# Performance work log

Measured on AMD Instinct MI355X. Metric: run time of the kernel, lower is better.

The kernel has to match this reference:

```python
import jax, jax.numpy as jnp
import numpy as np
import math

VOCAB = 32000
HIDDEN = 256
N_HEADS = 8
HEAD_DIM = 32
MAX_LEN = 2048


def _pos_encoding(max_len, d_model, dtype=jnp.float32):
    # Matches PositionalEncoding buffer (even d_model).
    pos = jnp.arange(max_len, dtype=dtype)[:, None]                       # [L,1]
    div = jnp.exp(jnp.arange(0, d_model, 2, dtype=dtype) * (-(math.log(10000.0) / d_model)))
    ang = pos * div                                                        # [L, d/2]
    pe = jnp.zeros((max_len, d_model), dtype=dtype)
    pe = pe.at[:, 0::2].set(jnp.sin(ang))
    pe = pe.at[:, 1::2].set(jnp.cos(ang))
    return pe


def setup_inputs() -> dict:
    key = jax.random.key(0)
    ks = jax.random.split(key, 7)
    B, S = 8, 2047
    s = 0.02
    x = jax.random.randint(ks[0], (B, S), 0, VOCAB + 1, dtype=jnp.int64)
    emb_w = jax.random.normal(ks[1], (VOCAB + 1, HIDDEN), jnp.float32) * s
    wq = jax.random.normal(ks[2], (N_HEADS, HEAD_DIM, HIDDEN), jnp.float32) * s
    wk = jax.random.normal(ks[3], (N_HEADS, HEAD_DIM, HIDDEN), jnp.float32) * s
    wv = jax.random.normal(ks[4], (N_HEADS, HEAD_DIM, HIDDEN), jnp.float32) * s
    wo = jax.random.normal(ks[5], (HIDDEN, N_HEADS * HEAD_DIM), jnp.float32) * s
    wu = jax.random.normal(ks[6], (VOCAB + 1, HIDDEN), jnp.float32) * s
    return {"x": x, "emb_w": emb_w, "wq": wq, "wk": wk, "wv": wv, "wo": wo, "wu": wu}


def reference(x, emb_w, wq, wk, wv, wo, wu):
    B, S = x.shape
    # prepend CLS token (id=2)
    tok = jnp.concatenate([jnp.full((B, 1), 2, dtype=x.dtype), x], axis=1)  # [B, S+1]
    y = emb_w[tok]                                                          # [B, S+1, H]
    y = y + _pos_encoding(S + 1, HIDDEN, y.dtype)
    # batched per-head QKV (nn.Linear: out = in @ W.T)
    q = jnp.einsum('bsh,nkh->bnsk', y, wq)
    k = jnp.einsum('bsh,nkh->bnsk', y, wk)
    v = jnp.einsum('bsh,nkh->bnsk', y, wv)
    scores = jnp.einsum('bnsk,bntk->bnst', q, k) / (HEAD_DIM ** 0.5)        # [B,N,S+1,S+1]
    A = jax.nn.softmax(scores, axis=-1)
    o = jnp.einsum('bnst,bntk->bnsk', A, v)                                 # [B,N,S+1,K]
    o = jnp.transpose(o, (0, 2, 1, 3)).reshape(B, S + 1, N_HEADS * HEAD_DIM)
    att = o @ wo.T + y     # residual inside MultiHeadAttention
    y = att + y            # second residual in MultiHeadTransformerPosEmb.forward
    out = y[:, 0, :] @ wu.T                                                 # [B, VOCAB+1]
    return out
```

## Files before the change

kernel.cpp:

```cpp
#include <hip/hip_runtime.h>
#include <stdint.h>

#define B_   8
#define S_   2047
#define L_   2048
#define H_   256
#define NH_  8
#define HD_  32
#define V_   32001
#define NCH_ 64
#define TCH_ 32

__device__ __forceinline__ float b2f(unsigned short u) {
    union { uint32_t i; float f; } c; c.i = ((uint32_t)u) << 16; return c.f;
}
__device__ __forceinline__ unsigned short f2b(float f) {
    union { float f; uint32_t i; } c; c.f = f;
    uint32_t x = c.i;
    uint32_t r = (x + 0x7fffu + ((x >> 16) & 1u)) >> 16;
    return (unsigned short)r;
}
__device__ __forceinline__ float foldx(float a, int off) {
    return a + __shfl_xor(a, off, 64);
}
__device__ __forceinline__ float sel8(const float a[8], int j) {
    float v = a[0];
    v = (j == 1) ? a[1] : v;
    v = (j == 2) ? a[2] : v;
    v = (j == 3) ? a[3] : v;
    v = (j == 4) ? a[4] : v;
    v = (j == 5) ? a[5] : v;
    v = (j == 6) ? a[6] : v;
    v = (j == 7) ? a[7] : v;
    return v;
}

__global__ __launch_bounds__(256) void k0_prep(const float* __restrict__ emb,
                                               const float* __restrict__ wq,
                                               const float* __restrict__ wk,
                                               float* __restrict__ qk,
                                               float* __restrict__ y0) {
    __shared__ float y0_l[H_];
    __shared__ float q0p[HD_][8];
    __shared__ float q0_l[HD_];
    int n = blockIdx.x, tid = threadIdx.x;
    float v = emb[2 * H_ + tid] + ((tid & 1) ? 1.0f : 0.0f);
    y0_l[tid] = v;
    if (n == 0) y0[tid] = v;
    __syncthreads();
    {
        int k = tid >> 3, part = tid & 7;
        const float* w = wq + (n * HD_ + k) * H_ + part * 32;
        const float* yy = y0_l + part * 32;
        float acc = 0.f;
#pragma unroll
        for (int j = 0; j < 32; ++j) acc += w[j] * yy[j];
        q0p[k][part] = acc;
    }
    __syncthreads();
    if (tid < HD_) {
        float s = 0.f;
#pragma unroll
        for (int j = 0; j < 8; ++j) s += q0p[tid][j];
        q0_l[tid] = s;
    }
    __syncthreads();
    float acc = 0.f;
    for (int k = 0; k < HD_; ++k)
        acc += q0_l[k] * wk[(n * HD_ + k) * H_ + tid];
    qk[n * H_ + tid] = acc * 0.17677669529663687f;
}

__global__ __launch_bounds__(256) void k1_scores(const int* __restrict__ x,
                                                 const float* __restrict__ emb,
                                                 const float* __restrict__ qkw,
                                                 unsigned short* __restrict__ ycache,
                                                 float* __restrict__ Et) {
    int tid  = threadIdx.x;
    int lane = tid & 63;
    int gid  = blockIdx.x * 4 + (tid >> 6);
    int b = gid >> 11, t = gid & (L_ - 1);
    int h0 = lane * 4;

    float4 qr[NH_];
#pragma unroll
    for (int n = 0; n < NH_; ++n)
        qr[n] = *(const float4*)(qkw + n * H_ + h0);

    const float cdiv = 0.07195578414202881f;
    float div0 = __expf(-(float)(lane * 2) * cdiv);
    float div1 = __expf(-(float)(lane * 2 + 1) * cdiv);
    float a0 = (float)t * div0, a1 = (float)t * div1;
    float s0 = __sinf(a0), c0 = __cosf(a0);
    float s1 = __sinf(a1), c1 = __cosf(a1);

    int tok = (t == 0) ? 2 : x[b * S_ + t - 1];
    float4 ev = *(const float4*)(emb + (size_t)tok * H_ + h0);
    float4 y4;
    y4.x = ev.x + s0; y4.y = ev.y + c0; y4.z = ev.z + s1; y4.w = ev.w + c1;
    ushort4 st;
    st.x = f2b(y4.x); st.y = f2b(y4.y); st.z = f2b(y4.z); st.w = f2b(y4.w);
    *(ushort4*)(ycache + ((size_t)gid << 8) + h0) = st;

    float a[NH_];
#pragma unroll
    for (int n = 0; n < NH_; ++n)
        a[n] = qr[n].x * y4.x + qr[n].y * y4.y + qr[n].z * y4.z + qr[n].w * y4.w;
    float m4[4];
#pragma unroll
    for (int k = 0; k < 4; ++k) {
        float lo = foldx(a[k], 32), hi = foldx(a[k + 4], 32);
        m4[k] = (lane & 32) ? hi : lo;
    }
    float m2[2];
#pragma unroll
    for (int k = 0; k < 2; ++k) {
        float lo = foldx(m4[k], 16), hi = foldx(m4[k + 2], 16);
        m2[k] = (lane & 16) ? hi : lo;
    }
    float lo = foldx(m2[0], 8), hi = foldx(m2[1], 8);
    float m1 = (lane & 8) ? hi : lo;
    m1 = foldx(m1, 4); m1 = foldx(m1, 2); m1 = foldx(m1, 1);
    float e = __expf(m1);
    if ((lane & 7) == 0)
        Et[(size_t)gid * NH_ + (lane >> 3)] = e;
}

__global__ __launch_bounds__(256) void k3_ybar(const float* __restrict__ Et,
                                               const unsigned short* __restrict__ ycache,
                                               float* __restrict__ psum,
                                               float* __restrict__ esum_blk) {
    int bid = blockIdx.x;
    int b = bid >> 6, c = bid & 63;
    int t0 = c * TCH_;
    int tid = threadIdx.x;

    __shared__ float e_l[TCH_ * NH_];
    e_l[tid] = Et[(size_t)(b * L_ + t0) * NH_ + tid];
    __syncthreads();
    if (tid < NH_) {
        float s = 0.f;
#pragma unroll
        for (int tt = 0; tt < TCH_; ++tt) s += e_l[tt * NH_ + tid];
        esum_blk[bid * NH_ + tid] = s;
    }

    float acc[NH_] = {};
    const unsigned short* yb = ycache + ((size_t)(b * L_ + t0) << 8) + tid;
#pragma unroll
    for (int tt = 0; tt < TCH_; ++tt) {
        float yv = b2f(yb[(size_t)tt << 8]);
        float4 eA = *(const float4*)&e_l[tt * NH_];
        float4 eB = *(const float4*)&e_l[tt * NH_ + 4];
        acc[0] += eA.x * yv; acc[1] += eA.y * yv;
        acc[2] += eA.z * yv; acc[3] += eA.w * yv;
        acc[4] += eB.x * yv; acc[5] += eB.y * yv;
        acc[6] += eB.z * yv; acc[7] += eB.w * yv;
    }
#pragma unroll
    for (int n = 0; n < NH_; ++n)
        psum[((size_t)bid * NH_ + n) * H_ + tid] = acc[n];
}

__global__ __launch_bounds__(256) void k4_heads(const float* __restrict__ psum,
                                                const float* __restrict__ esum_blk,
                                                const float* __restrict__ wv,
                                                float* __restrict__ o_g) {
    int bid = blockIdx.x; int b = bid >> 3, n = bid & 7;
    int tid = threadIdx.x;
    __shared__ float inv_s;
    __shared__ float ybar_l[H_];
    __shared__ float op[HD_][8];
    if (tid < 64) {
        float v = esum_blk[(b * NCH_ + tid) * NH_ + n];
#pragma unroll
        for (int off = 32; off > 0; off >>= 1) v += __shfl_xor(v, off, 64);
        if (tid == 0) inv_s = 1.0f / v;
    }
    __syncthreads();
    {
        const float* pp = psum + ((size_t)(b * NCH_) * NH_ + n) * H_ + tid;
        float s = 0.f;
#pragma unroll 8
        for (int cc = 0; cc < NCH_; ++cc) s += pp[(size_t)cc * NH_ * H_];
        ybar_l[tid] = s * inv_s;
    }
    __syncthreads();
    {
        int k = tid >> 3, p = tid & 7;
        const float* wrow = wv + (size_t)(n * HD_ + k) * H_ + p * 32;
        const float* yy = ybar_l + p * 32;
        float s = 0.f;
#pragma unroll
        for (int j = 0; j < 32; ++j) s += wrow[j] * yy[j];
        op[k][p] = s;
    }
    __syncthreads();
    if (tid < HD_) {
        float s = 0.f;
#pragma unroll
        for (int p = 0; p < 8; ++p) s += op[tid][p];
        o_g[b * (NH_ * HD_) + n * HD_ + tid] = s;
    }
}

__global__ __launch_bounds__(256) void k4b_z(const float* __restrict__ o_g,
                                             const float* __restrict__ wo,
                                             const float* __restrict__ y0,
                                             float* __restrict__ z) {
    int b = blockIdx.x, tid = threadIdx.x;
    __shared__ float o_l[NH_ * HD_];
    o_l[tid] = o_g[b * (NH_ * HD_) + tid];
    __syncthreads();
    const float* wrow = wo + (size_t)tid * (NH_ * HD_);
    float s = 0.f;
#pragma unroll 16
    for (int j4 = 0; j4 < (NH_ * HD_) / 4; ++j4) {
        float4 w4 = *(const float4*)(wrow + j4 * 4);
        s += w4.x * o_l[j4 * 4] + w4.y * o_l[j4 * 4 + 1]
           + w4.z * o_l[j4 * 4 + 2] + w4.w * o_l[j4 * 4 + 3];
    }
    z[b * H_ + tid] = s + 2.0f * y0[tid];
}

__global__ __launch_bounds__(256) void k5_out(const float* __restrict__ z,
                                              const float* __restrict__ wu,
                                              float* __restrict__ out) {
    int tid = threadIdx.x, lane = tid & 63, w = tid >> 6;
    int m = lane & 15;
    int g = lane >> 4;
    int hb = m * 16;
    float zr[B_][16];
#pragma unroll
    for (int b = 0; b < B_; ++b)
#pragma unroll
        for (int jj = 0; jj < 4; ++jj)
            *(float4*)&zr[b][jj * 4] = *(const float4*)(z + b * H_ + hb + jj * 4);

    __shared__ float o_l[B_ * 65];
    int base = blockIdx.x * 64;
#pragma unroll
    for (int pass = 0; pass < 4; ++pass) {
        int rl = w * 16 + pass * 4 + g;
        int v = base + rl;
        int vc = (v < V_) ? v : (V_ - 1);
        const float* wr = wu + (size_t)vc * H_ + hb;
        float4 w0 = *(const float4*)(wr);
        float4 w1 = *(const float4*)(wr + 4);
        float4 w2 = *(const float4*)(wr + 8);
        float4 w3 = *(const float4*)(wr + 12);
        float acc[B_];
#pragma unroll
        for (int b = 0; b < B_; ++b) {
            acc[b] = zr[b][0] * w0.x + zr[b][1] * w0.y + zr[b][2] * w0.z + zr[b][3] * w0.w
                   + zr[b][4] * w1.x + zr[b][5] * w1.y + zr[b][6] * w1.z + zr[b][7] * w1.w
                   + zr[b][8] * w2.x + zr[b][9] * w2.y + zr[b][10] * w2.z + zr[b][11] * w2.w
                   + zr[b][12] * w3.x + zr[b][13] * w3.y + zr[b][14] * w3.z + zr[b][15] * w3.w;
        }
#pragma unroll
        for (int off = 1; off <= 8; off <<= 1) {
#pragma unroll
            for (int b = 0; b < B_; ++b) acc[b] += __shfl_xor(acc[b], off, 64);
        }
        if (m < B_) o_l[m * 65 + rl] = sel8(acc, m);
    }
    __syncthreads();
    for (int i = tid; i < B_ * 64; i += 256) {
        int b = i >> 6, vl = i & 63, v = base + vl;
        if (v < V_) out[b * V_ + v] = o_l[b * 65 + vl];
    }
}

extern "C" void kernel_launch(void* const* d_in, const int* in_sizes, int n_in,
                              void* d_out, int out_size, void* d_ws, size_t ws_size,
                              hipStream_t stream) {
    const int*   x   = (const int*)d_in[0];
    const float* emb = (const float*)d_in[1];
    const float* wq  = (const float*)d_in[2];
    const float* wk  = (const float*)d_in[3];
    const float* wv  = (const float*)d_in[4];
    const float* wo  = (const float*)d_in[5];
    const float* wu  = (const float*)d_in[6];
    float*       out = (float*)d_out;

    float* qk       = (float*)d_ws;
    float* y0       = qk + NH_ * H_;
    float* z        = y0 + H_;
    float* o_g      = z + B_ * H_;
    float* esum_blk = o_g + NH_ * HD_ * B_;
    float* psum     = esum_blk + 512 * NH_;
    float* Et       = psum + (size_t)512 * NH_ * H_;
    unsigned short* ycache = (unsigned short*)(Et + (size_t)B_ * L_ * NH_);

    k0_prep  <<<8,    256, 0, stream>>>(emb, wq, wk, qk, y0);
    k1_scores<<<4096, 256, 0, stream>>>(x, emb, qk, ycache, Et);
    k3_ybar  <<<512,  256, 0, stream>>>(Et, ycache, psum, esum_blk);
    k4_heads <<<64,   256, 0, stream>>>(psum, esum_blk, wv, o_g);
    k4b_z    <<<8,    256, 0, stream>>>(o_g, wo, y0, z);
    k5_out   <<<(V_ + 63) / 64, 256, 0, stream>>>(z, wu, out);
}
```

Baseline: 163.1 us.

## Fuse score computation and weighted y-sum into one kernel, dropping y cache

Merges the per-token score kernel and the exp-weighted y reduction into a single kernel. Each block handles 32 tokens and each wave handles 8 of them. Embeddings plus positional encoding are recomputed in registers and accumulated directly, with a shared-memory reduction across waves. This removes the global write and read of the bf16 y cache and the exp-score buffer, and one kernel launch. The trade-off is fewer blocks, more per-thread work and larger shared memory use. Dropping the bf16 round trip on y also slightly changes numerics.

```diff
diff --git a/kernel.cpp b/kernel.cpp
--- a/kernel.cpp
+++ b/kernel.cpp
@@ -11,15 +11,6 @@
 #define NCH_ 64
 #define TCH_ 32
 
-__device__ __forceinline__ float b2f(unsigned short u) {
-    union { uint32_t i; float f; } c; c.i = ((uint32_t)u) << 16; return c.f;
-}
-__device__ __forceinline__ unsigned short f2b(float f) {
-    union { float f; uint32_t i; } c; c.f = f;
-    uint32_t x = c.i;
-    uint32_t r = (x + 0x7fffu + ((x >> 16) & 1u)) >> 16;
-    return (unsigned short)r;
-}
 __device__ __forceinline__ float foldx(float a, int off) {
     return a + __shfl_xor(a, off, 64);
 }
@@ -71,95 +62,104 @@
     qk[n * H_ + tid] = acc * 0.17677669529663687f;
 }
 
-__global__ __launch_bounds__(256) void k1_scores(const int* __restrict__ x,
-                                                 const float* __restrict__ emb,
-                                                 const float* __restrict__ qkw,
-                                                 unsigned short* __restrict__ ycache,
-                                                 float* __restrict__ Et) {
-    int tid  = threadIdx.x;
-    int lane = tid & 63;
-    int gid  = blockIdx.x * 4 + (tid >> 6);
-    int b = gid >> 11, t = gid & (L_ - 1);
+__global__ __launch_bounds__(256) void kB_scores_ybar(const int* __restrict__ x,
+                                                      const float* __restrict__ emb,
+                                                      const float* __restrict__ qkw,
+                                                      float* __restrict__ psum,
+                                                      float* __restrict__ esum_blk) {
+    int bid = blockIdx.x;
+    int b = bid >> 6, c = bid & 63;
+    int tid = threadIdx.x, lane = tid & 63, w = tid >> 6;
     int h0 = lane * 4;
 
+    __shared__ float qk_l[NH_ * H_];
+    __shared__ float red[4][NH_ * H_];
+    __shared__ float es_l[4][NH_];
+
+    for (int i = tid; i < (NH_ * H_) / 4; i += 256)
+        *(float4*)&qk_l[i * 4] = *(const float4*)(qkw + i * 4);
+    __syncthreads();
+
     float4 qr[NH_];
 #pragma unroll
     for (int n = 0; n < NH_; ++n)
-        qr[n] = *(const float4*)(qkw + n * H_ + h0);
+        qr[n] = *(const float4*)&qk_l[n * H_ + h0];
 
     const float cdiv = 0.07195578414202881f;
     float div0 = __expf(-(float)(lane * 2) * cdiv);
     float div1 = __expf(-(float)(lane * 2 + 1) * cdiv);
-    float a0 = (float)t * div0, a1 = (float)t * div1;
-    float s0 = __sinf(a0), c0 = __cosf(a0);
-    float s1 = __sinf(a1), c1 = __cosf(a1);
-
-    int tok = (t == 0) ? 2 : x[b * S_ + t - 1];
-    float4 ev = *(const float4*)(emb + (size_t)tok * H_ + h0);
-    float4 y4;
-    y4.x = ev.x + s0; y4.y = ev.y + c0; y4.z = ev.z + s1; y4.w = ev.w + c1;
-    ushort4 st;
-    st.x = f2b(y4.x); st.y = f2b(y4.y); st.z = f2b(y4.z); st.w = f2b(y4.w);
-    *(ushort4*)(ycache + ((size_t)gid << 8) + h0) = st;
-
-    float a[NH_];
+
+    float4 acc[NH_];
+    float es[NH_];
+#pragma unroll
+    for (int n = 0; n < NH_; ++n) {
+        acc[n] = make_float4(0.f, 0.f, 0.f, 0.f);
+        es[n] = 0.f;
+    }
+
+    int t0 = c * TCH_ + w * 8;
+    int toks[8];
+#pragma unroll
+    for (int i = 0; i < 8; ++i) {
+        int t = t0 + i;
+        toks[i] = (t == 0) ? 2 : x[b * S_ + t - 1];
+    }
+
+#pragma unroll
+    for (int i = 0; i < 8; ++i) {
+        int t = t0 + i;
+        float4 ev = *(const float4*)(emb + (size_t)toks[i] * H_ + h0);
+        float a0 = (float)t * div0, a1 = (float)t * div1;
+        float4 y4;
+        y4.x = ev.x + __sinf(a0); y4.y = ev.y + __cosf(a0);
+        y4.z = ev.z + __sinf(a1); y4.w = ev.w + __cosf(a1);
+
+        float a[NH_];
+#pragma unroll
+        for (int n = 0; n < NH_; ++n)
+            a[n] = qr[n].x * y4.x + qr[n].y * y4.y + qr[n].z * y4.z + qr[n].w * y4.w;
+
+        float m4[4];
+#pragma unroll
+        for (int k = 0; k < 4; ++k) {
+            float lo = foldx(a[k], 32), hi = foldx(a[k + 4], 32);
+            m4[k] = (lane & 32) ? hi : lo;
+        }
+        float m2[2];
+#pragma unroll
+        for (int k = 0; k < 2; ++k) {
+            float lo = foldx(m4[k], 16), hi = foldx(m4[k + 2], 16);
+            m2[k] = (lane & 16) ? hi : lo;
+        }
+        float lo = foldx(m2[0], 8), hi = foldx(m2[1], 8);
+        float m1 = (lane & 8) ? hi : lo;
+        m1 = foldx(m1, 4); m1 = foldx(m1, 2); m1 = foldx(m1, 1);
+        float e = __expf(m1);
+
+#pragma unroll
+        for (int n = 0; n < NH_; ++n) {
+            float en = __shfl(e, n * 8, 64);
+            acc[n].x += en * y4.x; acc[n].y += en * y4.y;
+            acc[n].z += en * y4.z; acc[n].w += en * y4.w;
+            es[n] += en;
+        }
+    }
+
 #pragma unroll
     for (int n = 0; n < NH_; ++n)
-        a[n] = qr[n].x * y4.x + qr[n].y * y4.y + qr[n].z * y4.z + qr[n].w * y4.w;
-    float m4[4];
-#pragma unroll
-    for (int k = 0; k < 4; ++k) {
-        float lo = foldx(a[k], 32), hi = foldx(a[k + 4], 32);
-        m4[k] = (lane & 32) ? hi : lo;
-    }
-    float m2[2];
-#pragma unroll
-    for (int k = 0; k < 2; ++k) {
-        float lo = foldx(m4[k], 16), hi = foldx(m4[k + 2], 16);
-        m2[k] = (lane & 16) ? hi : lo;
-    }
-    float lo = foldx(m2[0], 8), hi = foldx(m2[1], 8);
-    float m1 = (lane & 8) ? hi : lo;
-    m1 = foldx(m1, 4); m1 = foldx(m1, 2); m1 = foldx(m1, 1);
-    float e = __expf(m1);
-    if ((lane & 7) == 0)
-        Et[(size_t)gid * NH_ + (lane >> 3)] = e;
-}
-
-__global__ __launch_bounds__(256) void k3_ybar(const float* __restrict__ Et,
-                                               const unsigned short* __restrict__ ycache,
-                                               float* __restrict__ psum,
-                                               float* __restrict__ esum_blk) {
-    int bid = blockIdx.x;
-    int b = bid >> 6, c = bid & 63;
-    int t0 = c * TCH_;
-    int tid = threadIdx.x;
-
-    __shared__ float e_l[TCH_ * NH_];
-    e_l[tid] = Et[(size_t)(b * L_ + t0) * NH_ + tid];
-    __syncthreads();
-    if (tid < NH_) {
-        float s = 0.f;
-#pragma unroll
-        for (int tt = 0; tt < TCH_; ++tt) s += e_l[tt * NH_ + tid];
-        esum_blk[bid * NH_ + tid] = s;
-    }
-
-    float acc[NH_] = {};
-    const unsigned short* yb = ycache + ((size_t)(b * L_ + t0) << 8) + tid;
-#pragma unroll
-    for (int tt = 0; tt < TCH_; ++tt) {
-        float yv = b2f(yb[(size_t)tt << 8]);
-        float4 eA = *(const float4*)&e_l[tt * NH_];
-        float4 eB = *(const float4*)&e_l[tt * NH_ + 4];
-        acc[0] += eA.x * yv; acc[1] += eA.y * yv;
-        acc[2] += eA.z * yv; acc[3] += eA.w * yv;
-        acc[4] += eB.x * yv; acc[5] += eB.y * yv;
-        acc[6] += eB.z * yv; acc[7] += eB.w * yv;
-    }
-#pragma unroll
-    for (int n = 0; n < NH_; ++n)
-        psum[((size_t)bid * NH_ + n) * H_ + tid] = acc[n];
+        *(float4*)&red[w][n * H_ + h0] = acc[n];
+    if (lane < NH_) es_l[w][lane] = sel8(es, lane);
+    __syncthreads();
+
+#pragma unroll
+    for (int jj = 0; jj < (NH_ * H_) / 256; ++jj) {
+        int j = jj * 256 + tid;
+        psum[(size_t)bid * (NH_ * H_) + j] =
+            red[0][j] + red[1][j] + red[2][j] + red[3][j];
+    }
+    if (tid < NH_)
+        esum_blk[bid * NH_ + tid] =
+            es_l[0][tid] + es_l[1][tid] + es_l[2][tid] + es_l[3][tid];
 }
 
 __global__ __launch_bounds__(256) void k4_heads(const float* __restrict__ psum,
@@ -289,13 +289,10 @@
     float* o_g      = z + B_ * H_;
     float* esum_blk = o_g + NH_ * HD_ * B_;
     float* psum     = esum_blk + 512 * NH_;
-    float* Et       = psum + (size_t)512 * NH_ * H_;
-    unsigned short* ycache = (unsigned short*)(Et + (size_t)B_ * L_ * NH_);
-
-    k0_prep  <<<8,    256, 0, stream>>>(emb, wq, wk, qk, y0);
-    k1_scores<<<4096, 256, 0, stream>>>(x, emb, qk, ycache, Et);
-    k3_ybar  <<<512,  256, 0, stream>>>(Et, ycache, psum, esum_blk);
-    k4_heads <<<64,   256, 0, stream>>>(psum, esum_blk, wv, o_g);
-    k4b_z    <<<8,    256, 0, stream>>>(o_g, wo, y0, z);
-    k5_out   <<<(V_ + 63) / 64, 256, 0, stream>>>(z, wu, out);
-}
+
+    k0_prep       <<<8,   256, 0, stream>>>(emb, wq, wk, qk, y0);
+    kB_scores_ybar<<<512, 256, 0, stream>>>(x, emb, qk, psum, esum_blk);
+    k4_heads      <<<64,  256, 0, stream>>>(psum, esum_blk, wv, o_g);
+    k4b_z         <<<8,   256, 0, stream>>>(o_g, wo, y0, z);
+    k5_out        <<<(V_ + 63) / 64, 256, 0, stream>>>(z, wu, out);
+}
```

Result: slower. 185.0 us (+13.5%).

## Fuse all stages into one persistent megakernel with atomic grid barriers

Applied to the files above, without the earlier changes.

Replaces the six separate kernel launches with a single persistent kernel of 512 blocks. A hierarchical atomic-counter grid barrier separates the stages, and the score stage now loops over its work items. The aim is to remove per-launch gaps and tails between the small dependent stages. In exchange it adds a memset, barrier spin costs and a deadlock risk if the 512 blocks cannot all be resident at once.

```diff
diff --git a/kernel.cpp b/kernel.cpp
--- a/kernel.cpp
+++ b/kernel.cpp
@@ -10,6 +10,7 @@
 #define V_   32001
 #define NCH_ 64
 #define TCH_ 32
+#define GRID_ 512
 
 __device__ __forceinline__ float b2f(unsigned short u) {
     union { uint32_t i; float f; } c; c.i = ((uint32_t)u) << 16; return c.f;
@@ -35,239 +36,259 @@
     return v;
 }
 
-__global__ __launch_bounds__(256) void k0_prep(const float* __restrict__ emb,
+__device__ __forceinline__ void gsync(unsigned int* bp, int bid) {
+    __syncthreads();
+    if (threadIdx.x == 0) {
+        __threadfence();
+        unsigned int* sub = bp + 16 + (bid & 15) * 16;
+        unsigned int prev = atomicAdd(sub, 1u);
+        if (prev == (GRID_ / 16) - 1)
+            atomicAdd(bp, 1u);
+        while (__hip_atomic_load(bp, __ATOMIC_RELAXED, __HIP_MEMORY_SCOPE_AGENT) < 16u)
+            __builtin_amdgcn_s_sleep(1);
+        __threadfence();
+    }
+    __syncthreads();
+}
+
+__global__ __launch_bounds__(256, 2) void mega(const int* __restrict__ x,
+                                               const float* __restrict__ emb,
                                                const float* __restrict__ wq,
                                                const float* __restrict__ wk,
+                                               const float* __restrict__ wv,
+                                               const float* __restrict__ wo,
+                                               const float* __restrict__ wu,
+                                               float* __restrict__ out,
                                                float* __restrict__ qk,
-                                               float* __restrict__ y0) {
-    __shared__ float y0_l[H_];
-    __shared__ float q0p[HD_][8];
-    __shared__ float q0_l[HD_];
-    int n = blockIdx.x, tid = threadIdx.x;
-    float v = emb[2 * H_ + tid] + ((tid & 1) ? 1.0f : 0.0f);
-    y0_l[tid] = v;
-    if (n == 0) y0[tid] = v;
-    __syncthreads();
+                                               float* __restrict__ y0,
+                                               float* __restrict__ z,
+                                               float* __restrict__ o_g,
+                                               float* __restrict__ esum_blk,
+                                               float* __restrict__ psum,
+                                               float* __restrict__ Et,
+                                               unsigned short* __restrict__ ycache,
+                                               unsigned int* __restrict__ bars) {
+    int bid = blockIdx.x, tid = threadIdx.x;
+
+    __shared__ float sm_y0l[H_];
+    __shared__ float sm_p8[HD_][8];
+    __shared__ float sm_v32[HD_];
+    __shared__ float sm_e[TCH_ * NH_];
+    __shared__ float sm_ybar[H_];
+    __shared__ float sm_inv;
+    __shared__ float sm_o256[NH_ * HD_];
+    __shared__ float sm_out[B_ * 65];
+
+    if (bid < NH_) {
+        int n = bid;
+        float v = emb[2 * H_ + tid] + ((tid & 1) ? 1.0f : 0.0f);
+        sm_y0l[tid] = v;
+        if (n == 0) y0[tid] = v;
+        __syncthreads();
+        {
+            int k = tid >> 3, part = tid & 7;
+            const float* w = wq + (n * HD_ + k) * H_ + part * 32;
+            const float* yy = sm_y0l + part * 32;
+            float acc = 0.f;
+#pragma unroll
+            for (int j = 0; j < 32; ++j) acc += w[j] * yy[j];
+            sm_p8[k][part] = acc;
+        }
+        __syncthreads();
+        if (tid < HD_) {
+            float s = 0.f;
+#pragma unroll
+            for (int j = 0; j < 8; ++j) s += sm_p8[tid][j];
+            sm_v32[tid] = s;
+        }
+        __syncthreads();
+        float acc = 0.f;
+        for (int k = 0; k < HD_; ++k)
+            acc += sm_v32[k] * wk[(n * HD_ + k) * H_ + tid];
+        qk[n * H_ + tid] = acc * 0.17677669529663687f;
+    }
+    gsync(bars + 0 * 512, bid);
+
     {
-        int k = tid >> 3, part = tid & 7;
-        const float* w = wq + (n * HD_ + k) * H_ + part * 32;
-        const float* yy = y0_l + part * 32;
-        float acc = 0.f;
-#pragma unroll
-        for (int j = 0; j < 32; ++j) acc += w[j] * yy[j];
-        q0p[k][part] = acc;
-    }
-    __syncthreads();
-    if (tid < HD_) {
+        int lane = tid & 63;
+        int h0 = lane * 4;
+        float4 qr[NH_];
+#pragma unroll
+        for (int n = 0; n < NH_; ++n)
+            qr[n] = *(const float4*)(qk + n * H_ + h0);
+
+        const float cdiv = 0.07195578414202881f;
+        float div0 = __expf(-(float)(lane * 2) * cdiv);
+        float div1 = __expf(-(float)(lane * 2 + 1) * cdiv);
+
+        for (int g = bid; g < 4096; g += GRID_) {
+            int gid = g * 4 + (tid >> 6);
+            int b = gid >> 11, t = gid & (L_ - 1);
+
+            float a0 = (float)t * div0, a1 = (float)t * div1;
+            float s0 = __sinf(a0), c0 = __cosf(a0);
+            float s1 = __sinf(a1), c1 = __cosf(a1);
+
+            int tok = (t == 0) ? 2 : x[b * S_ + t - 1];
+            float4 ev = *(const float4*)(emb + (size_t)tok * H_ + h0);
+            float4 y4;
+            y4.x = ev.x + s0; y4.y = ev.y + c0; y4.z = ev.z + s1; y4.w = ev.w + c1;
+            ushort4 st;
+            st.x = f2b(y4.x); st.y = f2b(y4.y); st.z = f2b(y4.z); st.w = f2b(y4.w);
+            *(ushort4*)(ycache + ((size_t)gid << 8) + h0) = st;
+
+            float a[NH_];
+#pragma unroll
+            for (int n = 0; n < NH_; ++n)
+                a[n] = qr[n].x * y4.x + qr[n].y * y4.y + qr[n].z * y4.z + qr[n].w * y4.w;
+            float m4[4];
+#pragma unroll
+            for (int k = 0; k < 4; ++k) {
+                float lo = foldx(a[k], 32), hi = foldx(a[k + 4], 32);
+                m4[k] = (lane & 32) ? hi : lo;
+            }
+            float m2[2];
+#pragma unroll
+            for (int k = 0; k < 2; ++k) {
+                float lo = foldx(m4[k], 16), hi = foldx(m4[k + 2], 16);
+                m2[k] = (lane & 16) ? hi : lo;
+            }
+            float lo = foldx(m2[0], 8), hi = foldx(m2[1], 8);
+            float m1 = (lane & 8) ? hi : lo;
+            m1 = foldx(m1, 4); m1 = foldx(m1, 2); m1 = foldx(m1, 1);
+            float e = __expf(m1);
+            if ((lane & 7) == 0)
+                Et[(size_t)gid * NH_ + (lane >> 3)] = e;
+        }
+    }
+    gsync(bars + 1 * 512, bid);
+
+    {
+        int b = bid >> 6, c = bid & 63;
+        int t0 = c * TCH_;
+
+        sm_e[tid] = Et[(size_t)(b * L_ + t0) * NH_ + tid];
+        __syncthreads();
+        if (tid < NH_) {
+            float s = 0.f;
+#pragma unroll
+            for (int tt = 0; tt < TCH_; ++tt) s += sm_e[tt * NH_ + tid];
+            esum_blk[bid * NH_ + tid] = s;
+        }
+
+        float acc[NH_] = {};
+        const unsigned short* yb = ycache + ((size_t)(b * L_ + t0) << 8) + tid;
+#pragma unroll
+        for (int tt = 0; tt < TCH_; ++tt) {
+            float yv = b2f(yb[(size_t)tt << 8]);
+            float4 eA = *(const float4*)&sm_e[tt * NH_];
+            float4 eB = *(const float4*)&sm_e[tt * NH_ + 4];
+            acc[0] += eA.x * yv; acc[1] += eA.y * yv;
+            acc[2] += eA.z * yv; acc[3] += eA.w * yv;
+            acc[4] += eB.x * yv; acc[5] += eB.y * yv;
+            acc[6] += eB.z * yv; acc[7] += eB.w * yv;
+        }
+#pragma unroll
+        for (int n = 0; n < NH_; ++n)
+            psum[((size_t)bid * NH_ + n) * H_ + tid] = acc[n];
+    }
+    gsync(bars + 2 * 512, bid);
+
+    if (bid < 64) {
+        int b = bid >> 3, n = bid & 7;
+        if (tid < 64) {
+            float v = esum_blk[(b * NCH_ + tid) * NH_ + n];
+#pragma unroll
+            for (int off = 32; off > 0; off >>= 1) v += __shfl_xor(v, off, 64);
+            if (tid == 0) sm_inv = 1.0f / v;
+        }
+        __syncthreads();
+        {
+            const float* pp = psum + ((size_t)(b * NCH_) * NH_ + n) * H_ + tid;
+            float s = 0.f;
+#pragma unroll 8
+            for (int cc = 0; cc < NCH_; ++cc) s += pp[(size_t)cc * NH_ * H_];
+            sm_ybar[tid] = s * sm_inv;
+        }
+        __syncthreads();
+        {
+            int k = tid >> 3, p = tid & 7;
+            const float* wrow = wv + (size_t)(n * HD_ + k) * H_ + p * 32;
+            const float* yy = sm_ybar + p * 32;
+            float s = 0.f;
+#pragma unroll
+            for (int j = 0; j < 32; ++j) s += wrow[j] * yy[j];
+            sm_p8[k][p] = s;
+        }
+        __syncthreads();
+        if (tid < HD_) {
+            float s = 0.f;
+#pragma unroll
+            for (int p = 0; p < 8; ++p) s += sm_p8[tid][p];
+            o_g[b * (NH_ * HD_) + n * HD_ + tid] = s;
+        }
+    }
+    gsync(bars + 3 * 512, bid);
+
+    if (bid < B_) {
+        int b = bid;
+        sm_o256[tid] = o_g[b * (NH_ * HD_) + tid];
+        __syncthreads();
+        const float* wrow = wo + (size_t)tid * (NH_ * HD_);
         float s = 0.f;
-#pragma unroll
-        for (int j = 0; j < 8; ++j) s += q0p[tid][j];
-        q0_l[tid] = s;
-    }
-    __syncthreads();
-    float acc = 0.f;
-    for (int k = 0; k < HD_; ++k)
-        acc += q0_l[k] * wk[(n * HD_ + k) * H_ + tid];
-    qk[n * H_ + tid] = acc * 0.17677669529663687f;
-}
-
-__global__ __launch_bounds__(256) void k1_scores(const int* __restrict__ x,
-                                                 const float* __restrict__ emb,
-                                                 const float* __restrict__ qkw,
-                                                 unsigned short* __restrict__ ycache,
-                                                 float* __restrict__ Et) {
-    int tid  = threadIdx.x;
-    int lane = tid & 63;
-    int gid  = blockIdx.x * 4 + (tid >> 6);
-    int b = gid >> 11, t = gid & (L_ - 1);
-    int h0 = lane * 4;
-
-    float4 qr[NH_];
-#pragma unroll
-    for (int n = 0; n < NH_; ++n)
-        qr[n] = *(const float4*)(qkw + n * H_ + h0);
-
-    const float cdiv = 0.07195578414202881f;
-    float div0 = __expf(-(float)(lane * 2) * cdiv);
-    float div1 = __expf(-(float)(lane * 2 + 1) * cdiv);
-    float a0 = (float)t * div0, a1 = (float)t * div1;
-    float s0 = __sinf(a0), c0 = __cosf(a0);
-    float s1 = __sinf(a1), c1 = __cosf(a1);
-
-    int tok = (t == 0) ? 2 : x[b * S_ + t - 1];
-    float4 ev = *(const float4*)(emb + (size_t)tok * H_ + h0);
-    float4 y4;
-    y4.x = ev.x + s0; y4.y = ev.y + c0; y4.z = ev.z + s1; y4.w = ev.w + c1;
-    ushort4 st;
-    st.x = f2b(y4.x); st.y = f2b(y4.y); st.z = f2b(y4.z); st.w = f2b(y4.w);
-    *(ushort4*)(ycache + ((size_t)gid << 8) + h0) = st;
-
-    float a[NH_];
-#pragma unroll
-    for (int n = 0; n < NH_; ++n)
-        a[n] = qr[n].x * y4.x + qr[n].y * y4.y + qr[n].z * y4.z + qr[n].w * y4.w;
-    float m4[4];
-#pragma unroll
-    for (int k = 0; k < 4; ++k) {
-        float lo = foldx(a[k], 32), hi = foldx(a[k + 4], 32);
-        m4[k] = (lane & 32) ? hi : lo;
-    }
-    float m2[2];
-#pragma unroll
-    for (int k = 0; k < 2; ++k) {
-        float lo = foldx(m4[k], 16), hi = foldx(m4[k + 2], 16);
-        m2[k] = (lane & 16) ? hi : lo;
-    }
-    float lo = foldx(m2[0], 8), hi = foldx(m2[1], 8);
-    float m1 = (lane & 8) ? hi : lo;
-    m1 = foldx(m1, 4); m1 = foldx(m1, 2); m1 = foldx(m1, 1);
-    float e = __expf(m1);
-    if ((lane & 7) == 0)
-        Et[(size_t)gid * NH_ + (lane >> 3)] = e;
-}
-
-__global__ __launch_bounds__(256) void k3_ybar(const float* __restrict__ Et,
-                                               const unsigned short* __restrict__ ycache,
-                                               float* __restrict__ psum,
-                                               float* __restrict__ esum_blk) {
-    int bid = blockIdx.x;
-    int b = bid >> 6, c = bid & 63;
-    int t0 = c * TCH_;
-    int tid = threadIdx.x;
-
-    __shared__ float e_l[TCH_ * NH_];
-    e_l[tid] = Et[(size_t)(b * L_ + t0) * NH_ + tid];
-    __syncthreads();
-    if (tid < NH_) {
-        float s = 0.f;
-#pragma unroll
-        for (int tt = 0; tt < TCH_; ++tt) s += e_l[tt * NH_ + tid];
-        esum_blk[bid * NH_ + tid] = s;
-    }
-
-    float acc[NH_] = {};
-    const unsigned short* yb = ycache + ((size_t)(b * L_ + t0) << 8) + tid;
-#pragma unroll
-    for (int tt = 0; tt < TCH_; ++tt) {
-        float yv = b2f(yb[(size_t)tt << 8]);
-        float4 eA = *(const float4*)&e_l[tt * NH_];
-        float4 eB = *(const float4*)&e_l[tt * NH_ + 4];
-        acc[0] += eA.x * yv; acc[1] += eA.y * yv;
-        acc[2] += eA.z * yv; acc[3] += eA.w * yv;
-        acc[4] += eB.x * yv; acc[5] += eB.y * yv;
-        acc[6] += eB.z * yv; acc[7] += eB.w * yv;
-    }
-#pragma unroll
-    for (int n = 0; n < NH_; ++n)
-        psum[((size_t)bid * NH_ + n) * H_ + tid] = acc[n];
-}
-
-__global__ __launch_bounds__(256) void k4_heads(const float* __restrict__ psum,
-                                                const float* __restrict__ esum_blk,
-                                                const float* __restrict__ wv,
-                                                float* __restrict__ o_g) {
-    int bid = blockIdx.x; int b = bid >> 3, n = bid & 7;
-    int tid = threadIdx.x;
-    __shared__ float inv_s;
-    __shared__ float ybar_l[H_];
-    __shared__ float op[HD_][8];
-    if (tid < 64) {
-        float v = esum_blk[(b * NCH_ + tid) * NH_ + n];
-#pragma unroll
-        for (int off = 32; off > 0; off >>= 1) v += __shfl_xor(v, off, 64);
-        if (tid == 0) inv_s = 1.0f / v;
-    }
-    __syncthreads();
-    {
-        const float* pp = psum + ((size_t)(b * NCH_) * NH_ + n) * H_ + tid;
-        float s = 0.f;
-#pragma unroll 8
-        for (int cc = 0; cc < NCH_; ++cc) s += pp[(size_t)cc * NH_ * H_];
-        ybar_l[tid] = s * inv_s;
-    }
-    __syncthreads();
-    {
-        int k = tid >> 3, p = tid & 7;
-        const float* wrow = wv + (size_t)(n * HD_ + k) * H_ + p * 32;
-        const float* yy = ybar_l + p * 32;
-        float s = 0.f;
-#pragma unroll
-        for (int j = 0; j < 32; ++j) s += wrow[j] * yy[j];
-        op[k][p] = s;
-    }
-    __syncthreads();
-    if (tid < HD_) {
-        float s = 0.f;
-#pragma unroll
-        for (int p = 0; p < 8; ++p) s += op[tid][p];
-        o_g[b * (NH_ * HD_) + n * HD_ + tid] = s;
-    }
-}
-
-__global__ __launch_bounds__(256) void k4b_z(const float* __restrict__ o_g,
-                                             const float* __restrict__ wo,
-                                             const float* __restrict__ y0,
-                                             float* __restrict__ z) {
-    int b = blockIdx.x, tid = threadIdx.x;
-    __shared__ float o_l[NH_ * HD_];
-    o_l[tid] = o_g[b * (NH_ * HD_) + tid];
-    __syncthreads();
-    const float* wrow = wo + (size_t)tid * (NH_ * HD_);
-    float s = 0.f;
 #pragma unroll 16
-    for (int j4 = 0; j4 < (NH_ * HD_) / 4; ++j4) {
-        float4 w4 = *(const float4*)(wrow + j4 * 4);
-        s += w4.x * o_l[j4 * 4] + w4.y * o_l[j4 * 4 + 1]
-           + w4.z * o_l[j4 * 4 + 2] + w4.w * o_l[j4 * 4 + 3];
-    }
-    z[b * H_ + tid] = s + 2.0f * y0[tid];
-}
-
-__global__ __launch_bounds__(256) void k5_out(const float* __restrict__ z,
-                                              const float* __restrict__ wu,
-                                              float* __restrict__ out) {
-    int tid = threadIdx.x, lane = tid & 63, w = tid >> 6;
-    int m = lane & 15;
-    int g = lane >> 4;
-    int hb = m * 16;
-    float zr[B_][16];
-#pragma unroll
-    for (int b = 0; b < B_; ++b)
-#pragma unroll
-        for (int jj = 0; jj < 4; ++jj)
-            *(float4*)&zr[b][jj * 4] = *(const float4*)(z + b * H_ + hb + jj * 4);
-
-    __shared__ float o_l[B_ * 65];
-    int base = blockIdx.x * 64;
-#pragma unroll
-    for (int pass = 0; pass < 4; ++pass) {
-        int rl = w * 16 + pass * 4 + g;
-        int v = base + rl;
-        int vc = (v < V_) ? v : (V_ - 1);
-        const float* wr = wu + (size_t)vc * H_ + hb;
-        float4 w0 = *(const float4*)(wr);
-        float4 w1 = *(const float4*)(wr + 4);
-        float4 w2 = *(const float4*)(wr + 8);
-        float4 w3 = *(const float4*)(wr + 12);
-        float acc[B_];
-#pragma unroll
-        for (int b = 0; b < B_; ++b) {
-            acc[b] = zr[b][0] * w0.x + zr[b][1] * w0.y + zr[b][2] * w0.z + zr[b][3] * w0.w
-                   + zr[b][4] * w1.x + zr[b][5] * w1.y + zr[b][6] * w1.z + zr[b][7] * w1.w
-                   + zr[b][8] * w2.x + zr[b][9] * w2.y + zr[b][10] * w2.z + zr[b][11] * w2.w
-                   + zr[b][12] * w3.x + zr[b][13] * w3.y + zr[b][14] * w3.z + zr[b][15] * w3.w;
-        }
-#pragma unroll
-        for (int off = 1; off <= 8; off <<= 1) {
-#pragma unroll
-            for (int b = 0; b < B_; ++b) acc[b] += __shfl_xor(acc[b], off, 64);
-        }
-        if (m < B_) o_l[m * 65 + rl] = sel8(acc, m);
-    }
-    __syncthreads();
-    for (int i = tid; i < B_ * 64; i += 256) {
-        int b = i >> 6, vl = i & 63, v = base + vl;
-        if (v < V_) out[b * V_ + v] = o_l[b * 65 + vl];
+        for (int j4 = 0; j4 < (NH_ * HD_) / 4; ++j4) {
+            float4 w4 = *(const float4*)(wrow + j4 * 4);
+            s += w4.x * sm_o256[j4 * 4] + w4.y * sm_o256[j4 * 4 + 1]
+               + w4.z * sm_o256[j4 * 4 + 2] + w4.w * sm_o256[j4 * 4 + 3];
+        }
+        z[b * H_ + tid] = s + 2.0f * y0[tid];
+    }
+    gsync(bars + 4 * 512, bid);
+
+    if (bid < (V_ + 63) / 64) {
+        int lane = tid & 63, w = tid >> 6;
+        int m = lane & 15;
+        int g = lane >> 4;
+        int hb = m * 16;
+        float zr[B_][16];
+#pragma unroll
+        for (int b = 0; b < B_; ++b)
+#pragma unroll
+            for (int jj = 0; jj < 4; ++jj)
+                *(float4*)&zr[b][jj * 4] = *(const float4*)(z + b * H_ + hb + jj * 4);
+
+        int base = bid * 64;
+#pragma unroll
+        for (int pass = 0; pass < 4; ++pass) {
+            int rl = w * 16 + pass * 4 + g;
+            int v = base + rl;
+            int vc = (v < V_) ? v : (V_ - 1);
+            const float* wr = wu + (size_t)vc * H_ + hb;
+            float4 w0 = *(const float4*)(wr);
+            float4 w1 = *(const float4*)(wr + 4);
+            float4 w2 = *(const float4*)(wr + 8);
+            float4 w3 = *(const float4*)(wr + 12);
+            float acc[B_];
+#pragma unroll
+            for (int b = 0; b < B_; ++b) {
+                acc[b] = zr[b][0] * w0.x + zr[b][1] * w0.y + zr[b][2] * w0.z + zr[b][3] * w0.w
+                       + zr[b][4] * w1.x + zr[b][5] * w1.y + zr[b][6] * w1.z + zr[b][7] * w1.w
+                       + zr[b][8] * w2.x + zr[b][9] * w2.y + zr[b][10] * w2.z + zr[b][11] * w2.w
+                       + zr[b][12] * w3.x + zr[b][13] * w3.y + zr[b][14] * w3.z + zr[b][15] * w3.w;
+            }
+#pragma unroll
+            for (int off = 1; off <= 8; off <<= 1) {
+#pragma unroll
+                for (int b = 0; b < B_; ++b) acc[b] += __shfl_xor(acc[b], off, 64);
+            }
+            if (m < B_) sm_out[m * 65 + rl] = sel8(acc, m);
+        }
+        __syncthreads();
+        for (int i = tid; i < B_ * 64; i += 256) {
+            int b = i >> 6, vl = i & 63, v = base + vl;
+            if (v < V_) out[b * V_ + v] = sm_out[b * 65 + vl];
+        }
     }
 }
 
@@ -291,11 +312,10 @@
     float* psum     = esum_blk + 512 * NH_;
     float* Et       = psum + (size_t)512 * NH_ * H_;
     unsigned short* ycache = (unsigned short*)(Et + (size_t)B_ * L_ * NH_);
-
-    k0_prep  <<<8,    256, 0, stream>>>(emb, wq, wk, qk, y0);
-    k1_scores<<<4096, 256, 0, stream>>>(x, emb, qk, ycache, Et);
-    k3_ybar  <<<512,  256, 0, stream>>>(Et, ycache, psum, esum_blk);
-    k4_heads <<<64,   256, 0, stream>>>(psum, esum_blk, wv, o_g);
-    k4b_z    <<<8,    256, 0, stream>>>(o_g, wo, y0, z);
-    k5_out   <<<(V_ + 63) / 64, 256, 0, stream>>>(z, wu, out);
-}
+    unsigned int*   bars   = (unsigned int*)(ycache + (size_t)B_ * L_ * H_);
+
+    hipMemsetAsync(bars, 0, 5 * 512 * sizeof(unsigned int), stream);
+
+    mega<<<GRID_, 256, 0, stream>>>(x, emb, wq, wk, wv, wo, wu, out,
+                                    qk, y0, z, o_g, esum_blk, psum, Et, ycache, bars);
+}
```

New measurement: 261.7 us. +60.5%, slower.
